# Kernel tuning notes

Measured on AMD Instinct MI355X. Metric: run time of the kernel, lower is better.

Reference implementation:

```python
import jax, jax.numpy as jnp
import numpy as np

V, D, M, H, C = 100000, 300, 300, 200, 5
L = 512


def setup_inputs() -> dict:
    key = jax.random.key(0)
    ks = jax.random.split(key, 20)
    def rn(k, shape, s=0.05):
        return jax.random.normal(k, shape, dtype=jnp.float32) * s
    return {
        "linputs": jax.random.randint(ks[0], (L,), 0, V),
        "rinputs": jax.random.randint(ks[1], (L,), 0, V),
        "emb": rn(ks[2], (V, D), 0.1),
        "ioux_w": rn(ks[3], (3 * M, D)), "ioux_b": jnp.zeros((3 * M,), jnp.float32),
        "iouh_w": rn(ks[4], (3 * M, M)), "iouh_b": jnp.zeros((3 * M,), jnp.float32),
        "fx_w": rn(ks[5], (M, D)), "fx_b": jnp.zeros((M,), jnp.float32),
        "fh_w": rn(ks[6], (M, M)), "fh_b": jnp.zeros((M,), jnp.float32),
        "Wa": rn(ks[7], (1, M)),
        "attnh_w": rn(ks[8], (M, 2 * M)), "attnh_b": jnp.zeros((M,), jnp.float32),
        "wh_w": rn(ks[9], (H, 4 * M)), "wh_b": jnp.zeros((H,), jnp.float32),
        "wp_w": rn(ks[10], (C, H)), "wp_b": jnp.zeros((C,), jnp.float32),
    }


def _run_chain(inputs, hmat, ioux_w, ioux_b, iouh_w, iouh_b, fx_w, fx_b, fh_w, fh_b,
               Wa, attnh_w, attnh_b):
    """Sequential ChildSum tree-LSTM chain (each node's sole child is the previous node).
    inputs: [L, D]; hmat: None or [N, M] attention memory. Returns (c, h, hs[L,M])."""
    m = iouh_w.shape[1]

    def step(carry, x):
        c, h = carry  # each [1, M]
        iou = (x @ ioux_w.T + ioux_b) + (h @ iouh_w.T + iouh_b)  # [1, 3M]
        i_, o_, u_ = jnp.split(iou, 3, axis=1)
        i_, o_, u_ = jax.nn.sigmoid(i_), jax.nn.sigmoid(o_), jnp.tanh(u_)
        f = jax.nn.sigmoid((h @ fh_w.T + fh_b) + (x @ fx_w.T + fx_b))  # [1, M]
        c_new = i_ * u_ + f * c  # sum over single child == identity
        h_new = o_ * jnp.tanh(c_new)
        if hmat is not None:
            n = hmat.shape[0]
            cat = jnp.concatenate([jnp.broadcast_to(h_new, (n, m)), hmat], axis=1)  # [N, 2M]
            scores = Wa @ jnp.tanh(cat @ attnh_w.T + attnh_b).T  # [1, N]
            s = jax.nn.softmax(scores, axis=1)  # [1, N]
            h_new = (jnp.sum((1.0 - s).T * hmat, axis=0, keepdims=True)
                     + jnp.sum(s.T * jnp.broadcast_to(h_new, (n, m)), axis=0, keepdims=True))
        return (c_new, h_new), h_new[0]

    init = (jnp.zeros((1, m), inputs.dtype), jnp.zeros((1, m), inputs.dtype))
    (c, h), hs = jax.lax.scan(step, init, inputs)
    return c, h, hs  # hs: [L, M]


def _forward(linputs, rinputs, emb, ioux_w, ioux_b, iouh_w, iouh_b, fx_w, fx_b,
             fh_w, fh_b, Wa, attnh_w, attnh_b, wh_w, wh_b, wp_w, wp_b):
    cell = (ioux_w, ioux_b, iouh_w, iouh_b, fx_w, fx_b, fh_w, fh_b, Wa, attnh_w, attnh_b)
    lemb = emb[linputs]          # [L, D]
    remb = emb[rinputs]          # [R, D]
    lflip = lemb[::-1]
    rflip = remb[::-1]

    # left, no attention (runs 1)
    _, lh_f1, hs_l_f = _run_chain(lemb, None, *cell)
    _, _, hs_l_b = _run_chain(lflip, None, *cell)
    lh_b1 = hs_l_b[0:1]
    lhidden_1 = jnp.concatenate([lh_f1, lh_b1], axis=1)  # [1, 2M]
    hs_l = jnp.tanh(hs_l_f + hs_l_b[::-1])               # [L, M]

    # right, attention over left hidden states
    _, rh_f1, _ = _run_chain(remb, hs_l, *cell)
    _, _, hs_tmp = _run_chain(rflip, hs_l, *cell)
    rh_b1 = hs_tmp[0:1]
    rhidden_1 = jnp.concatenate([rh_f1, rh_b1], axis=1)

    # right, no attention (runs 2)
    _, rh_f2, hs_r_f = _run_chain(remb, None, *cell)
    _, _, hs_r_b = _run_chain(rflip, None, *cell)
    rh_b2 = hs_r_b[0:1]
    rhidden_2 = jnp.concatenate([rh_f2, rh_b2], axis=1)
    hs_r = jnp.tanh(hs_r_f + hs_r_b[::-1])

    # left, attention over right hidden states
    _, lh_f2, _ = _run_chain(lemb, hs_r, *cell)
    _, _, hs_tmp2 = _run_chain(lflip, hs_r, *cell)
    lh_b2 = hs_tmp2[0:1]
    lhidden_2 = jnp.concatenate([lh_f2, lh_b2], axis=1)

    lhidden = jnp.tanh(lhidden_1 + lhidden_2)  # [1, 2M]
    rhidden = jnp.tanh(rhidden_1 + rhidden_2)

    mult_dist = lhidden * rhidden
    abs_dist = jnp.abs(lhidden - rhidden)
    vec_dist = jnp.concatenate([mult_dist, abs_dist], axis=1)  # [1, 4M]
    hid = jax.nn.sigmoid(vec_dist @ wh_w.T + wh_b)             # [1, H]
    return jax.nn.log_softmax(hid @ wp_w.T + wp_b, axis=1)     # [1, C]


def reference(linputs, rinputs, emb, ioux_w, ioux_b, iouh_w, iouh_b, fx_w, fx_b,
              fh_w, fh_b, Wa, attnh_w, attnh_b, wh_w, wh_b, wp_w, wp_b):
    return _forward(linputs, rinputs, emb, ioux_w, ioux_b, iouh_w, iouh_b,
                    fx_w, fx_b, fh_w, fh_b, Wa, attnh_w, attnh_b,
                    wh_w, wh_b, wp_w, wp_b)
```

## Files before the change

kernel.cpp:

```cpp
#include <hip/hip_runtime.h>
#include <hip/hip_bf16.h>

constexpr int kL = 512;
constexpr int kD = 300;
constexpr int kM = 300;
constexpr int NWG = 32;
constexpr int BLK = 256;
constexpr int JP = 10;
constexpr int NJW = 30;
constexpr int NSPLIT = 6;
constexpr int KLEN = 50;
constexpr int NSL = 16;
constexpr int SEG = 4;

constexpr int A_LEMB   = 1024;
constexpr int A_REMB   = A_LEMB   + kL*kD;
constexpr int A_XIOU_L = A_REMB   + kL*kD;
constexpr int A_XF_L   = A_XIOU_L + kL*900;
constexpr int A_XIOU_R = A_XF_L   + kL*300;
constexpr int A_XF_R   = A_XIOU_R + kL*900;
constexpr int A_HS_LF  = A_XF_R   + kL*300;
constexpr int A_HS_LB  = A_HS_LF  + kL*300;
constexpr int A_HS_RF  = A_HS_LB  + kL*300;
constexpr int A_HS_RB  = A_HS_RF  + kL*300;
constexpr int A_HS_L   = A_HS_RB  + kL*300;
constexpr int A_HS_R   = A_HS_L   + kL*300;
constexpr int A_HABUF  = A_HS_R   + kL*300;
constexpr int A_HBBUF  = A_HABUF  + 2400;
constexpr int A_HPACC  = A_HBBUF  + 2400;
constexpr int A_HACC   = A_HPACC  + 9600;
constexpr int A_DACC   = A_HACC   + 9600;
constexpr int A_BFIN   = A_DACC   + 256;
constexpr int A_END    = A_BFIN   + 1200;

__device__ __forceinline__ float fsig(float x) { return 1.0f / (1.0f + __expf(-x)); }
__device__ __forceinline__ float ftanh(float x) {
  x = fminf(fmaxf(x, -15.f), 15.f);
  float e = __expf(2.f * x);
  return (e - 1.f) / (e + 1.f);
}

__device__ __forceinline__ float aload(const float* p) {
  return __hip_atomic_load(p, __ATOMIC_RELAXED, __HIP_MEMORY_SCOPE_AGENT);
}
__device__ __forceinline__ void astore(float* p, float v) {
  __hip_atomic_store(p, v, __ATOMIC_RELAXED, __HIP_MEMORY_SCOPE_AGENT);
}

__device__ __forceinline__ void gbar(unsigned* ctr, int& epoch) {
  __syncthreads();
  if (threadIdx.x == 0) {
    ++epoch;
    __threadfence();
    atomicAdd(ctr, 1u);
    const unsigned tgt = (unsigned)(NWG * epoch);
    while (__hip_atomic_load(ctr, __ATOMIC_RELAXED, __HIP_MEMORY_SCOPE_AGENT) < tgt)
      __builtin_amdgcn_s_sleep(1);
    __threadfence();
  }
  __syncthreads();
}

__device__ __forceinline__ void gbar_fast(unsigned* ctr, int& epoch) {
  __syncthreads();
  if (threadIdx.x == 0) {
    ++epoch;
    atomicAdd(ctr, 1u);
    const unsigned tgt = (unsigned)(NWG * epoch);
    while (__hip_atomic_load(ctr, __ATOMIC_RELAXED, __HIP_MEMORY_SCOPE_AGENT) < tgt)
      __builtin_amdgcn_s_sleep(1);
  }
  __syncthreads();
}

__global__ __launch_bounds__(BLK) void treelstm_kernel(
    const int* __restrict__ linputs, const int* __restrict__ rinputs,
    const float* __restrict__ emb,
    const float* __restrict__ ioux_w, const float* __restrict__ ioux_b,
    const float* __restrict__ iouh_w, const float* __restrict__ iouh_b,
    const float* __restrict__ fx_w,  const float* __restrict__ fx_b,
    const float* __restrict__ fh_w,  const float* __restrict__ fh_b,
    const float* __restrict__ Wa,    const float* __restrict__ attnh_w,
    const float* __restrict__ attnh_b,
    const float* __restrict__ wh_w,  const float* __restrict__ wh_b,
    const float* __restrict__ wp_w,  const float* __restrict__ wp_b,
    float* __restrict__ ws, float* __restrict__ out) {

  __shared__ __align__(16) float h_lds[4][304];
  __shared__ __align__(16) float hpj_lds[4][304];
  __shared__ __align__(16) float part[4][40][6];
  __shared__ float gv[4][4][10];
  __shared__ float c_lds[4][10];
  __shared__ float hnew_lds[4][10];
  __shared__ float dred[4][32];
  __shared__ __align__(16) float colsum_lds[2][300];
  __shared__ float wa_lds[300];
  __shared__ float sc_lds[4][16];
  __shared__ float red_lds[32];
  __shared__ __align__(16) __hip_bfloat16 hmp_lds[2][NSL][300];
  __shared__ __align__(16) __hip_bfloat16 hmat_lds[2][NSL][300];
  __shared__ __hip_bfloat16 a1c_lds[JP][300];

  const int wg = blockIdx.x;
  const int tid = threadIdx.x;
  const int gthread = wg * BLK + tid;
  unsigned* ctr = (unsigned*)ws;
  float* W = ws;
  int epoch = 0;

  for (int i = gthread; i < 2 * kL * kD; i += NWG * BLK) {
    int side = i / (kL * kD); int r = i % (kL * kD); int t = r / kD; int d = r % kD;
    const int* idx = side ? rinputs : linputs;
    W[(side ? A_REMB : A_LEMB) + r] = emb[(long)idx[t] * kD + d];
  }
  for (int i = gthread; i < 4800; i += NWG * BLK) astore(&W[A_HABUF + i], 0.f);
  for (int i = gthread; i < 19200; i += NWG * BLK) astore(&W[A_HPACC + i], 0.f);
  gbar(ctr, epoch);

  for (int task = wg; task < 64; task += NWG) {
    int side = task & 1; int tb = task >> 1;
    float* xt = (float*)hmp_lds;
    const float* xbase = W + (side ? A_REMB : A_LEMB) + tb * 16 * kD;
    for (int i = tid; i < 16 * kD; i += BLK) xt[i] = xbase[i];
    __syncthreads();
    float* xiou = W + (side ? A_XIOU_R : A_XIOU_L) + tb * 16 * 900;
    float* xf   = W + (side ? A_XF_R   : A_XF_L)   + tb * 16 * 300;
    const float4* xt4 = (const float4*)xt;
    for (int id = tid; id < 1200; id += BLK) {
      int o4 = id >> 2, q = id & 3;
      int o0 = o4 * 4;
      float acc[4][4];
      const float* wrow[4]; float bias[4];
      #pragma unroll
      for (int m = 0; m < 4; ++m) {
        int o = o0 + m;
        if (o < 900) { wrow[m] = ioux_w + o * kD; bias[m] = ioux_b[o]; }
        else         { wrow[m] = fx_w + (o - 900) * kD; bias[m] = fx_b[o - 900]; }
        #pragma unroll
        for (int n = 0; n < 4; ++n) acc[m][n] = bias[m];
      }
      for (int k4 = 0; k4 < 75; ++k4) {
        float4 x4[4];
        #pragma unroll
        for (int n = 0; n < 4; ++n) x4[n] = xt4[(q * 4 + n) * 75 + k4];
        #pragma unroll
        for (int m = 0; m < 4; ++m) {
          float4 w4 = *(const float4*)(wrow[m] + k4 * 4);
          #pragma unroll
          for (int n = 0; n < 4; ++n)
            acc[m][n] += w4.x * x4[n].x + w4.y * x4[n].y + w4.z * x4[n].z + w4.w * x4[n].w;
        }
      }
      #pragma unroll
      for (int m = 0; m < 4; ++m) {
        int o = o0 + m;
        #pragma unroll
        for (int n = 0; n < 4; ++n) {
          int tt = q * 4 + n;
          if (o < 900) xiou[tt * 900 + o] = acc[m][n];
          else         xf[tt * 300 + (o - 900)] = acc[m][n];
        }
      }
    }
    __syncthreads();
  }
  gbar(ctr, epoch);

  float wreg[KLEN];
  int r6 = 0, s6 = 0, k0 = 0;
  if (wg < NJW && tid < 240) {
    r6 = tid / NSPLIT; s6 = tid % NSPLIT;
    int gate = r6 / JP, jl = r6 % JP, jg = wg * JP + jl;
    k0 = s6 * KLEN;
    const float* wrow = (gate < 3) ? (iouh_w + (gate * kM + jg) * kM) : (fh_w + jg * kM);
    #pragma unroll
    for (int k = 0; k < KLEN; ++k) wreg[k] = wrow[k0 + k];
  }
  float biasr = 0.f; int ach = 0, ag = 0, ajl = 0, ajg = 0;
  if (wg < NJW && tid < 160) {
    ach = tid / 40; ag = (tid / 10) % 4; ajl = tid % 10; ajg = wg * JP + ajl;
    biasr = (ag < 3) ? iouh_b[ag * kM + ajg] : fh_b[ajg];
  }
  int gch = 0, gjl = 0, gjg = 0;
  if (wg < NJW && tid < 40) { gch = tid / 10; gjl = tid % 10; gjg = wg * JP + gjl; }

  if (tid < 40) c_lds[tid / 10][tid % 10] = 0.f;
  __syncthreads();

  int p = 0;
  for (int t = 0; t < kL; ++t) {
    for (int i = tid; i < 1200; i += BLK)
      h_lds[i / 300][i % 300] = aload(&W[A_HABUF + p * 1200 + i]);
    float xv = 0.f;
    if (wg < NJW && tid < 160) {
      int trow = (ach & 1) ? (511 - t) : t;
      if (ag < 3) xv = W[(ach < 2 ? A_XIOU_L : A_XIOU_R) + trow * 900 + ag * 300 + ajg];
      else        xv = W[(ach < 2 ? A_XF_L   : A_XF_R)   + trow * 300 + ajg];
    }
    __syncthreads();
    if (wg < NJW && tid < 240) {
      #pragma unroll
      for (int ch = 0; ch < 4; ++ch) {
        float acc = 0.f;
        #pragma unroll
        for (int k = 0; k < KLEN; ++k) acc += wreg[k] * h_lds[ch][k0 + k];
        part[ch][r6][s6] = acc;
      }
    }
    __syncthreads();
    if (wg < NJW && tid < 160) {
      float pre = xv + biasr;
      #pragma unroll
      for (int s = 0; s < NSPLIT; ++s) pre += part[ach][ag * 10 + ajl][s];
      gv[ach][ag][ajl] = pre;
    }
    __syncthreads();
    if (wg < NJW && tid < 40) {
      float iv = fsig(gv[gch][0][gjl]);
      float ov = fsig(gv[gch][1][gjl]);
      float uv = ftanh(gv[gch][2][gjl]);
      float fv = fsig(gv[gch][3][gjl]);
      float c = iv * uv + fv * c_lds[gch][gjl];
      c_lds[gch][gjl] = c;
      float h = ov * ftanh(c);
      astore(&W[A_HABUF + (p ^ 1) * 1200 + gch * 300 + gjg], h);
      int hsoff = (gch == 0) ? A_HS_LF : (gch == 1) ? A_HS_LB : (gch == 2) ? A_HS_RF : A_HS_RB;
      astore(&W[hsoff + t * 300 + gjg], h);
    }
    gbar_fast(ctr, epoch);
    p ^= 1;
  }

  for (int i = gthread; i < 2 * kL * kM; i += NWG * BLK) {
    int side = i / (kL * kM); int r = i % (kL * kM); int n = r / kM; int j = r % kM;
    float v = ftanh(W[(side ? A_HS_RF : A_HS_LF) + n * kM + j] +
                    W[(side ? A_HS_RB : A_HS_LB) + (511 - n) * kM + j]);
    astore(&W[(side ? A_HS_R : A_HS_L) + n * kM + j], v);
  }
  gbar_fast(ctr, epoch);

  for (int j = tid; j < 300; j += BLK) wa_lds[j] = Wa[j];
  if (wg < NJW)
    for (int i = tid; i < JP * 300; i += BLK) {
      int kl = i / 300, j = i % 300;
      a1c_lds[kl][j] = __float2bfloat16(attnh_w[j * 600 + wg * JP + kl]);
    }
  for (int j = tid; j < 300; j += BLK) {
    float s0 = 0.f, s1 = 0.f;
    for (int n = 0; n < kL; ++n) { s0 += W[A_HS_L + n * 300 + j]; s1 += W[A_HS_R + n * 300 + j]; }
    colsum_lds[0][j] = s0; colsum_lds[1][j] = s1;
  }
  for (int side = 0; side < 2; ++side) {
    __syncthreads();
    float* stage = (float*)hmat_lds;
    for (int i = tid; i < NSL * 300; i += BLK)
      stage[i] = W[(side ? A_HS_R : A_HS_L) + (wg * NSL) * 300 + i];
    __syncthreads();
    const float4* st4 = (const float4*)stage;
    for (int id = tid; id < 1200; id += BLK) {
      int j = id >> 2, q = id & 3;
      float b = attnh_b[j];
      float acc[4] = {b, b, b, b};
      const float* wrow = attnh_w + j * 600 + 300;
      for (int k4 = 0; k4 < 75; ++k4) {
        float4 w4 = *(const float4*)(wrow + k4 * 4);
        #pragma unroll
        for (int m = 0; m < 4; ++m) {
          float4 x4 = st4[(q * 4 + m) * 75 + k4];
          acc[m] += w4.x * x4.x + w4.y * x4.y + w4.z * x4.z + w4.w * x4.w;
        }
      }
      #pragma unroll
      for (int m = 0; m < 4; ++m) hmp_lds[side][q * 4 + m][j] = __float2bfloat16(acc[m]);
    }
  }
  __syncthreads();
  for (int i = tid; i < 2 * NSL * 300; i += BLK) {
    int side = i / (NSL * 300); int r = i % (NSL * 300);
    hmat_lds[side][r / 300][r % 300] =
        __float2bfloat16(W[(side ? A_HS_R : A_HS_L) + (wg * NSL) * 300 + r]);
  }
  for (int i = tid; i < 1216; i += BLK) ((float*)h_lds)[i] = 0.f;
  if (tid < 40) c_lds[tid / 10][tid % 10] = 0.f;
  gbar_fast(ctr, epoch);

  int pb = 0;
  for (int t = 0; t < kL; ++t) {
    const int nact = (t == 0) ? 4 : 2;
    float xvb = 0.f;
    if (wg < NJW && tid < 160 && ach < nact) {
      int trow = (ach < 2) ? t : 511;
      int useL = ach & 1;
      if (ag < 3) xvb = W[(useL ? A_XIOU_L : A_XIOU_R) + trow * 900 + ag * 300 + ajg];
      else        xvb = W[(useL ? A_XF_L   : A_XF_R)   + trow * 300 + ajg];
    }
    __syncthreads();
    if (wg < NJW && tid < 240) {
      for (int ch = 0; ch < nact; ++ch) {
        float acc = 0.f;
        #pragma unroll
        for (int k = 0; k < KLEN; ++k) acc += wreg[k] * h_lds[ch][k0 + k];
        part[ch][r6][s6] = acc;
      }
    }
    __syncthreads();
    if (wg < NJW && tid < 160 && ach < nact) {
      float pre = xvb + biasr;
      #pragma unroll
      for (int s = 0; s < NSPLIT; ++s) pre += part[ach][ag * 10 + ajl][s];
      gv[ach][ag][ajl] = pre;
    }
    __syncthreads();
    if (wg < NJW && tid < 40 && gch < nact) {
      float iv = fsig(gv[gch][0][gjl]);
      float ov = fsig(gv[gch][1][gjl]);
      float uv = ftanh(gv[gch][2][gjl]);
      float fv = fsig(gv[gch][3][gjl]);
      float c = iv * uv + fv * c_lds[gch][gjl];
      c_lds[gch][gjl] = c;
      float h = ov * ftanh(c);
      astore(&W[A_HBBUF + pb * 1200 + gch * 300 + gjg], h);
      hnew_lds[gch][gjl] = h;
    }
    __syncthreads();
    if (wg < NJW) {
      for (int ch = 0; ch < nact; ++ch)
        for (int j = tid; j < 300; j += BLK) {
          float acc = 0.f;
          #pragma unroll
          for (int kl = 0; kl < JP; ++kl)
            acc += hnew_lds[ch][kl] * __bfloat162float(a1c_lds[kl][j]);
          atomicAdd(&W[A_HPACC + ((pb * SEG + (wg & 3)) * 4 + ch) * 300 + j], acc);
        }
    }
    gbar_fast(ctr, epoch);

    for (int i = tid; i < SEG * 4 * 300; i += BLK) astore(&W[A_HACC + (pb ^ 1) * 4800 + i], 0.f);
    for (int i = tid; i < nact * 300; i += BLK) {
      int ch = i / 300, j = i % 300;
      float s_ = 0.f;
      #pragma unroll
      for (int sg = 0; sg < SEG; ++sg) s_ += aload(&W[A_HPACC + ((pb * SEG + sg) * 4 + ch) * 300 + j]);
      hpj_lds[ch][j] = s_;
    }
    __syncthreads();
    float* pf = &part[0][0][0];
    for (int id = tid; id < nact * NSL * 8; id += BLK) {
      int ch = id / 128; int rem = id % 128; int nl = rem / 8; int js = rem % 8;
      int side = ch & 1;
      int j0 = js * 38; int j1 = j0 + 38; if (j1 > 300) j1 = 300;
      float acc = 0.f;
      for (int j = j0; j < j1; ++j)
        acc += wa_lds[j] * ftanh(hpj_lds[ch][j] + __bfloat162float(hmp_lds[side][nl][j]));
      pf[id] = acc;
    }
    __syncthreads();
    if (tid < nact * NSL) {
      int ch = tid / NSL, nl = tid % NSL;
      float sc = 0.f;
      #pragma unroll
      for (int js = 0; js < 8; ++js) sc += pf[(ch * NSL + nl) * 8 + js];
      sc = fminf(fmaxf(sc, -60.f), 60.f);
      sc_lds[ch][nl] = __expf(sc);
    }
    __syncthreads();
    if (tid < nact) {
      float dsum = 0.f;
      #pragma unroll
      for (int nl = 0; nl < NSL; ++nl) dsum += sc_lds[tid][nl];
      astore(&W[A_DACC + (pb * 32 + wg) * 4 + tid], dsum);
    }
    for (int ch = 0; ch < nact; ++ch) {
      int side = ch & 1;
      for (int j = tid; j < 300; j += BLK) {
        float acc = 0.f;
        #pragma unroll
        for (int nl = 0; nl < NSL; ++nl)
          acc += sc_lds[ch][nl] * __bfloat162float(hmat_lds[side][nl][j]);
        atomicAdd(&W[A_HACC + ((pb * SEG + (wg & 3)) * 4 + ch) * 300 + j], acc);
      }
    }
    gbar_fast(ctr, epoch);

    for (int i = tid; i < SEG * 4 * 300; i += BLK) astore(&W[A_HPACC + pb * 4800 + i], 0.f);
    if (tid < 32 * nact) {
      int ch = tid >> 5, w2 = tid & 31;
      dred[ch][w2] = aload(&W[A_DACC + (pb * 32 + w2) * 4 + ch]);
    }
    __syncthreads();
    if (tid < nact) {
      float den = 0.f;
      #pragma unroll
      for (int w2 = 0; w2 < NWG; ++w2) den += dred[tid][w2];
      gv[0][0][tid] = den;
    }
    __syncthreads();
    for (int ch = 0; ch < nact; ++ch) {
      float inv = 1.f / gv[0][0][ch];
      int side = ch & 1;
      for (int j = tid; j < 300; j += BLK) {
        float s_ = 0.f;
        #pragma unroll
        for (int sg = 0; sg < SEG; ++sg) s_ += aload(&W[A_HACC + ((pb * SEG + sg) * 4 + ch) * 300 + j]);
        float val = aload(&W[A_HBBUF + pb * 1200 + ch * 300 + j]) + colsum_lds[side][j] - s_ * inv;
        h_lds[ch][j] = val;
        if (t == 511 && ch == 0) astore(&W[A_BFIN + 0   + j], val);
        if (t == 511 && ch == 1) astore(&W[A_BFIN + 600 + j], val);
        if (t == 0   && ch == 2) astore(&W[A_BFIN + 300 + j], val);
        if (t == 0   && ch == 3) astore(&W[A_BFIN + 900 + j], val);
      }
    }
    __syncthreads();
    pb ^= 1;
  }
  gbar_fast(ctr, epoch);

  if (wg == 0) {
    float* hl = (float*)h_lds;
    float* vec = (float*)hpj_lds;
    float* hid = &part[0][0][0];
    for (int j = tid; j < 300; j += BLK) {
      float lf = W[A_HS_LF + 511 * 300 + j] + aload(&W[A_BFIN + 600 + j]);
      float lb = W[A_HS_LB + j]             + aload(&W[A_BFIN + 900 + j]);
      float rf = aload(&W[A_BFIN + j])      + W[A_HS_RF + 511 * 300 + j];
      float rb = aload(&W[A_BFIN + 300 + j]) + W[A_HS_RB + j];
      hl[j]        = ftanh(lf);
      hl[300 + j]  = ftanh(lb);
      hl[608 + j]  = ftanh(rf);
      hl[908 + j]  = ftanh(rb);
    }
    __syncthreads();
    for (int i = tid; i < 600; i += BLK) {
      float a = hl[i], b = hl[608 + i];
      vec[i] = a * b; vec[600 + i] = fabsf(a - b);
    }
    __syncthreads();
    for (int hh = tid; hh < 200; hh += BLK) {
      float acc = wh_b[hh];
      const float* wr = wh_w + hh * 1200;
      for (int i2 = 0; i2 < 1200; ++i2) acc += wr[i2] * vec[i2];
      hid[hh] = fsig(acc);
    }
    __syncthreads();
    if (tid < 5) {
      float acc = wp_b[tid];
      const float* wr = wp_w + tid * 200;
      for (int h2 = 0; h2 < 200; ++h2) acc += wr[h2] * hid[h2];
      red_lds[tid] = acc;
    }
    __syncthreads();
    if (tid == 0) {
      float mx = red_lds[0];
      for (int c2 = 1; c2 < 5; ++c2) mx = fmaxf(mx, red_lds[c2]);
      float se = 0.f;
      for (int c2 = 0; c2 < 5; ++c2) se += __expf(red_lds[c2] - mx);
      float lse = logf(se) + mx;
      for (int c2 = 0; c2 < 5; ++c2) out[c2] = red_lds[c2] - lse;
    }
  }
}

extern "C" void kernel_launch(void* const* d_in, const int* in_sizes, int n_in,
                              void* d_out, int out_size, void* d_ws, size_t ws_size,
                              hipStream_t stream) {
  (void)in_sizes; (void)n_in; (void)out_size; (void)ws_size;
  hipMemsetAsync(d_ws, 0, 256, stream);
  treelstm_kernel<<<NWG, BLK, 0, stream>>>(
      (const int*)d_in[0], (const int*)d_in[1], (const float*)d_in[2],
      (const float*)d_in[3], (const float*)d_in[4], (const float*)d_in[5],
      (const float*)d_in[6], (const float*)d_in[7], (const float*)d_in[8],
      (const float*)d_in[9], (const float*)d_in[10], (const float*)d_in[11],
      (const float*)d_in[12], (const float*)d_in[13], (const float*)d_in[14],
      (const float*)d_in[15], (const float*)d_in[16], (const float*)d_in[17],
      (float*)d_ws, (float*)d_out);
}
```

Before: 10.10 ms.

## Replace grid barriers with tagged-value dataflow polling in recurrent loops

```diff
diff --git a/kernel.cpp b/kernel.cpp
--- a/kernel.cpp
+++ b/kernel.cpp
@@ -11,7 +11,6 @@
 constexpr int NSPLIT = 6;
 constexpr int KLEN = 50;
 constexpr int NSL = 16;
-constexpr int SEG = 4;
 
 constexpr int A_LEMB   = 1024;
 constexpr int A_REMB   = A_LEMB   + kL*kD;
@@ -25,13 +24,15 @@
 constexpr int A_HS_RB  = A_HS_RF  + kL*300;
 constexpr int A_HS_L   = A_HS_RB  + kL*300;
 constexpr int A_HS_R   = A_HS_L   + kL*300;
-constexpr int A_HABUF  = A_HS_R   + kL*300;
-constexpr int A_HBBUF  = A_HABUF  + 2400;
-constexpr int A_HPACC  = A_HBBUF  + 2400;
-constexpr int A_HACC   = A_HPACC  + 9600;
-constexpr int A_DACC   = A_HACC   + 9600;
-constexpr int A_BFIN   = A_DACC   + 256;
-constexpr int A_END    = A_BFIN   + 1200;
+constexpr int A_TAIL   = A_HS_R   + kL*300;
+
+constexpr int U_PJ  = A_LEMB / 2;
+constexpr int U_PV  = U_PJ + 2*30*4*300;
+constexpr int U_HXA = A_TAIL / 2;
+constexpr int U_HXB = U_HXA + 2*4*300;
+constexpr int U_HP  = U_HXB + 2*2*300;
+constexpr int U_DEN = U_HP  + 2*4*300;
+constexpr int A_BFIN = (U_DEN + 2*32*4) * 2;
 
 __device__ __forceinline__ float fsig(float x) { return 1.0f / (1.0f + __expf(-x)); }
 __device__ __forceinline__ float ftanh(float x) {
@@ -45,6 +46,15 @@
 }
 __device__ __forceinline__ void astore(float* p, float v) {
   __hip_atomic_store(p, v, __ATOMIC_RELAXED, __HIP_MEMORY_SCOPE_AGENT);
+}
+__device__ __forceinline__ unsigned long long uload(const unsigned long long* p) {
+  return __hip_atomic_load(p, __ATOMIC_RELAXED, __HIP_MEMORY_SCOPE_AGENT);
+}
+__device__ __forceinline__ void ustore(unsigned long long* p, unsigned long long v) {
+  __hip_atomic_store(p, v, __ATOMIC_RELAXED, __HIP_MEMORY_SCOPE_AGENT);
+}
+__device__ __forceinline__ unsigned long long pack(unsigned tag, float v) {
+  return ((unsigned long long)tag << 32) | (unsigned long long)__float_as_uint(v);
 }
 
 __device__ __forceinline__ void gbar(unsigned* ctr, int& epoch) {
@@ -60,7 +70,6 @@
   }
   __syncthreads();
 }
-
 __device__ __forceinline__ void gbar_fast(unsigned* ctr, int& epoch) {
   __syncthreads();
   if (threadIdx.x == 0) {
@@ -71,6 +80,26 @@
       __builtin_amdgcn_s_sleep(1);
   }
   __syncthreads();
+}
+
+__device__ __forceinline__ void poll_lds(const unsigned long long* src, float* lds,
+                                         int n, unsigned tag) {
+  int idx[5]; int cnt = 0;
+  for (int i = threadIdx.x; i < n; i += BLK) idx[cnt++] = i;
+  int rem = cnt;
+  while (rem > 0) {
+    #pragma unroll
+    for (int q = 0; q < 5; ++q) {
+      if (q < cnt && idx[q] >= 0) {
+        unsigned long long v = uload(&src[idx[q]]);
+        if ((unsigned)(v >> 32) == tag) {
+          int i = idx[q];
+          lds[(i / 300) * 304 + (i % 300)] = __uint_as_float((unsigned)v);
+          idx[q] = -1; --rem;
+        }
+      }
+    }
+  }
 }
 
 __global__ __launch_bounds__(BLK) void treelstm_kernel(
@@ -106,6 +135,8 @@
   const int gthread = wg * BLK + tid;
   unsigned* ctr = (unsigned*)ws;
   float* W = ws;
+  unsigned long long* Ux = (unsigned long long*)ws;
+  float (*part2)[6] = (float(*)[6])&part[0][0][0];
   int epoch = 0;
 
   for (int i = gthread; i < 2 * kL * kD; i += NWG * BLK) {
@@ -113,8 +144,8 @@
     const int* idx = side ? rinputs : linputs;
     W[(side ? A_REMB : A_LEMB) + r] = emb[(long)idx[t] * kD + d];
   }
-  for (int i = gthread; i < 4800; i += NWG * BLK) astore(&W[A_HABUF + i], 0.f);
-  for (int i = gthread; i < 19200; i += NWG * BLK) astore(&W[A_HPACC + i], 0.f);
+  for (int i = gthread; i < 1200; i += NWG * BLK)
+    ustore(&Ux[U_HXA + i], pack(0u, 0.f));
   gbar(ctr, epoch);
 
   for (int task = wg; task < 64; task += NWG) {
@@ -187,49 +218,49 @@
   if (tid < 40) c_lds[tid / 10][tid % 10] = 0.f;
   __syncthreads();
 
-  int p = 0;
-  for (int t = 0; t < kL; ++t) {
-    for (int i = tid; i < 1200; i += BLK)
-      h_lds[i / 300][i % 300] = aload(&W[A_HABUF + p * 1200 + i]);
-    float xv = 0.f;
-    if (wg < NJW && tid < 160) {
-      int trow = (ach & 1) ? (511 - t) : t;
-      if (ag < 3) xv = W[(ach < 2 ? A_XIOU_L : A_XIOU_R) + trow * 900 + ag * 300 + ajg];
-      else        xv = W[(ach < 2 ? A_XF_L   : A_XF_R)   + trow * 300 + ajg];
-    }
-    __syncthreads();
-    if (wg < NJW && tid < 240) {
-      #pragma unroll
-      for (int ch = 0; ch < 4; ++ch) {
-        float acc = 0.f;
-        #pragma unroll
-        for (int k = 0; k < KLEN; ++k) acc += wreg[k] * h_lds[ch][k0 + k];
-        part[ch][r6][s6] = acc;
-      }
-    }
-    __syncthreads();
-    if (wg < NJW && tid < 160) {
-      float pre = xv + biasr;
-      #pragma unroll
-      for (int s = 0; s < NSPLIT; ++s) pre += part[ach][ag * 10 + ajl][s];
-      gv[ach][ag][ajl] = pre;
-    }
-    __syncthreads();
-    if (wg < NJW && tid < 40) {
-      float iv = fsig(gv[gch][0][gjl]);
-      float ov = fsig(gv[gch][1][gjl]);
-      float uv = ftanh(gv[gch][2][gjl]);
-      float fv = fsig(gv[gch][3][gjl]);
-      float c = iv * uv + fv * c_lds[gch][gjl];
-      c_lds[gch][gjl] = c;
-      float h = ov * ftanh(c);
-      astore(&W[A_HABUF + (p ^ 1) * 1200 + gch * 300 + gjg], h);
-      int hsoff = (gch == 0) ? A_HS_LF : (gch == 1) ? A_HS_LB : (gch == 2) ? A_HS_RF : A_HS_RB;
-      astore(&W[hsoff + t * 300 + gjg], h);
-    }
-    gbar_fast(ctr, epoch);
-    p ^= 1;
-  }
+  if (wg < NJW) {
+    for (int t = 0; t < kL; ++t) {
+      float xv = 0.f;
+      if (tid < 160) {
+        int trow = (ach & 1) ? (511 - t) : t;
+        if (ag < 3) xv = W[(ach < 2 ? A_XIOU_L : A_XIOU_R) + trow * 900 + ag * 300 + ajg];
+        else        xv = W[(ach < 2 ? A_XF_L   : A_XF_R)   + trow * 300 + ajg];
+      }
+      poll_lds(&Ux[U_HXA + (t & 1) * 1200], &h_lds[0][0], 1200, (unsigned)t);
+      __syncthreads();
+      if (tid < 240) {
+        #pragma unroll
+        for (int ch = 0; ch < 4; ++ch) {
+          float acc = 0.f;
+          #pragma unroll
+          for (int k = 0; k < KLEN; ++k) acc += wreg[k] * h_lds[ch][k0 + k];
+          part[ch][r6][s6] = acc;
+        }
+      }
+      __syncthreads();
+      if (tid < 160) {
+        float pre = xv + biasr;
+        #pragma unroll
+        for (int s = 0; s < NSPLIT; ++s) pre += part[ach][ag * 10 + ajl][s];
+        gv[ach][ag][ajl] = pre;
+      }
+      __syncthreads();
+      if (tid < 40) {
+        float iv = fsig(gv[gch][0][gjl]);
+        float ov = fsig(gv[gch][1][gjl]);
+        float uv = ftanh(gv[gch][2][gjl]);
+        float fv = fsig(gv[gch][3][gjl]);
+        float c = iv * uv + fv * c_lds[gch][gjl];
+        c_lds[gch][gjl] = c;
+        float h = ov * ftanh(c);
+        ustore(&Ux[U_HXA + ((t + 1) & 1) * 1200 + gch * 300 + gjg],
+               pack((unsigned)(t + 1), h));
+        int hsoff = (gch == 0) ? A_HS_LF : (gch == 1) ? A_HS_LB : (gch == 2) ? A_HS_RF : A_HS_RB;
+        astore(&W[hsoff + t * 300 + gjg], h);
+      }
+    }
+  }
+  gbar_fast(ctr, epoch);
 
   for (int i = gthread; i < 2 * kL * kM; i += NWG * BLK) {
     int side = i / (kL * kM); int r = i % (kL * kM); int n = r / kM; int j = r % kM;
@@ -280,69 +311,93 @@
     hmat_lds[side][r / 300][r % 300] =
         __float2bfloat16(W[(side ? A_HS_R : A_HS_L) + (wg * NSL) * 300 + r]);
   }
-  for (int i = tid; i < 1216; i += BLK) ((float*)h_lds)[i] = 0.f;
   if (tid < 40) c_lds[tid / 10][tid % 10] = 0.f;
   gbar_fast(ctr, epoch);
 
-  int pb = 0;
   for (int t = 0; t < kL; ++t) {
     const int nact = (t == 0) ? 4 : 2;
-    float xvb = 0.f;
-    if (wg < NJW && tid < 160 && ach < nact) {
-      int trow = (ach < 2) ? t : 511;
-      int useL = ach & 1;
-      if (ag < 3) xvb = W[(useL ? A_XIOU_L : A_XIOU_R) + trow * 900 + ag * 300 + ajg];
-      else        xvb = W[(useL ? A_XF_L   : A_XF_R)   + trow * 300 + ajg];
-    }
-    __syncthreads();
-    if (wg < NJW && tid < 240) {
-      for (int ch = 0; ch < nact; ++ch) {
-        float acc = 0.f;
-        #pragma unroll
-        for (int k = 0; k < KLEN; ++k) acc += wreg[k] * h_lds[ch][k0 + k];
-        part[ch][r6][s6] = acc;
-      }
-    }
-    __syncthreads();
-    if (wg < NJW && tid < 160 && ach < nact) {
-      float pre = xvb + biasr;
-      #pragma unroll
-      for (int s = 0; s < NSPLIT; ++s) pre += part[ach][ag * 10 + ajl][s];
-      gv[ach][ag][ajl] = pre;
-    }
-    __syncthreads();
-    if (wg < NJW && tid < 40 && gch < nact) {
-      float iv = fsig(gv[gch][0][gjl]);
-      float ov = fsig(gv[gch][1][gjl]);
-      float uv = ftanh(gv[gch][2][gjl]);
-      float fv = fsig(gv[gch][3][gjl]);
-      float c = iv * uv + fv * c_lds[gch][gjl];
-      c_lds[gch][gjl] = c;
-      float h = ov * ftanh(c);
-      astore(&W[A_HBBUF + pb * 1200 + gch * 300 + gjg], h);
-      hnew_lds[gch][gjl] = h;
-    }
-    __syncthreads();
+    const unsigned tagS = (unsigned)(t + 1);
+    const int rows = nact * JP;
+    const int sl = t & 1;
+
     if (wg < NJW) {
-      for (int ch = 0; ch < nact; ++ch)
-        for (int j = tid; j < 300; j += BLK) {
+      float xvb = 0.f;
+      if (tid < 160 && ach < nact) {
+        int trow = (ach < 2) ? t : 511;
+        int useL = ach & 1;
+        if (ag < 3) xvb = W[(useL ? A_XIOU_L : A_XIOU_R) + trow * 900 + ag * 300 + ajg];
+        else        xvb = W[(useL ? A_XF_L   : A_XF_R)   + trow * 300 + ajg];
+      }
+      if (t == 0) {
+        for (int i = tid; i < 1216; i += BLK) ((float*)h_lds)[i] = 0.f;
+      } else {
+        poll_lds(&Ux[U_HXB + sl * 600], &h_lds[0][0], 600, (unsigned)t);
+      }
+      __syncthreads();
+      if (tid < 240) {
+        for (int ch = 0; ch < nact; ++ch) {
           float acc = 0.f;
           #pragma unroll
-          for (int kl = 0; kl < JP; ++kl)
-            acc += hnew_lds[ch][kl] * __bfloat162float(a1c_lds[kl][j]);
-          atomicAdd(&W[A_HPACC + ((pb * SEG + (wg & 3)) * 4 + ch) * 300 + j], acc);
-        }
-    }
-    gbar_fast(ctr, epoch);
-
-    for (int i = tid; i < SEG * 4 * 300; i += BLK) astore(&W[A_HACC + (pb ^ 1) * 4800 + i], 0.f);
-    for (int i = tid; i < nact * 300; i += BLK) {
-      int ch = i / 300, j = i % 300;
-      float s_ = 0.f;
-      #pragma unroll
-      for (int sg = 0; sg < SEG; ++sg) s_ += aload(&W[A_HPACC + ((pb * SEG + sg) * 4 + ch) * 300 + j]);
-      hpj_lds[ch][j] = s_;
-    }
+          for (int k = 0; k < KLEN; ++k) acc += wreg[k] * h_lds[ch][k0 + k];
+          part[ch][r6][s6] = acc;
+        }
+      }
+      __syncthreads();
+      if (tid < 160 && ach < nact) {
+        float pre = xvb + biasr;
+        #pragma unroll
+        for (int s = 0; s < NSPLIT; ++s) pre += part[ach][ag * 10 + ajl][s];
+        gv[ach][ag][ajl] = pre;
+      }
+      __syncthreads();
+      if (tid < 40 && gch < nact) {
+        float iv = fsig(gv[gch][0][gjl]);
+        float ov = fsig(gv[gch][1][gjl]);
+        float uv = ftanh(gv[gch][2][gjl]);
+        float fv = fsig(gv[gch][3][gjl]);
+        float c = iv * uv + fv * c_lds[gch][gjl];
+        c_lds[gch][gjl] = c;
+        hnew_lds[gch][gjl] = ov * ftanh(c);
+      }
+      __syncthreads();
+      for (int i = tid; i < nact * 300; i += BLK) {
+        int ch = i / 300, j = i % 300;
+        float acc = 0.f;
+        #pragma unroll
+        for (int kl = 0; kl < JP; ++kl)
+          acc += hnew_lds[ch][kl] * __bfloat162float(a1c_lds[kl][j]);
+        ustore(&Ux[U_PJ + sl * 36000 + wg * 1200 + ch * 300 + j], pack(tagS, acc));
+      }
+      if (tid < rows * 6) {
+        int r = tid / 6, l = tid % 6;
+        int ch = r / JP, jl = r % JP, jg = wg * JP + jl;
+        float acc = 0.f; unsigned pend = 0x1fu;
+        while (pend) {
+          #pragma unroll
+          for (int k = 0; k < 5; ++k) {
+            if (pend & (1u << k)) {
+              unsigned long long v =
+                  uload(&Ux[U_PJ + sl * 36000 + (l * 5 + k) * 1200 + ch * 300 + jg]);
+              if ((unsigned)(v >> 32) == tagS) {
+                acc += __uint_as_float((unsigned)v);
+                pend &= ~(1u << k);
+              }
+            }
+          }
+        }
+        part2[r][l] = acc;
+      }
+      __syncthreads();
+      if (tid < rows) {
+        float hp = 0.f;
+        #pragma unroll
+        for (int l = 0; l < 6; ++l) hp += part2[tid][l];
+        int ch = tid / JP, jl = tid % JP;
+        ustore(&Ux[U_HP + sl * 1200 + ch * 300 + wg * JP + jl], pack(tagS, hp));
+      }
+    }
+
+    poll_lds(&Ux[U_HP + sl * 1200], &hpj_lds[0][0], nact * 300, tagS);
     __syncthreads();
     float* pf = &part[0][0][0];
     for (int id = tid; id < nact * NSL * 8; id += BLK) {
@@ -368,50 +423,77 @@
       float dsum = 0.f;
       #pragma unroll
       for (int nl = 0; nl < NSL; ++nl) dsum += sc_lds[tid][nl];
-      astore(&W[A_DACC + (pb * 32 + wg) * 4 + tid], dsum);
-    }
-    for (int ch = 0; ch < nact; ++ch) {
+      ustore(&Ux[U_DEN + sl * 128 + wg * 4 + tid], pack(tagS, dsum));
+    }
+    for (int i = tid; i < nact * 300; i += BLK) {
+      int ch = i / 300, j = i % 300;
       int side = ch & 1;
-      for (int j = tid; j < 300; j += BLK) {
-        float acc = 0.f;
-        #pragma unroll
-        for (int nl = 0; nl < NSL; ++nl)
-          acc += sc_lds[ch][nl] * __bfloat162float(hmat_lds[side][nl][j]);
-        atomicAdd(&W[A_HACC + ((pb * SEG + (wg & 3)) * 4 + ch) * 300 + j], acc);
-      }
-    }
-    gbar_fast(ctr, epoch);
-
-    for (int i = tid; i < SEG * 4 * 300; i += BLK) astore(&W[A_HPACC + pb * 4800 + i], 0.f);
-    if (tid < 32 * nact) {
-      int ch = tid >> 5, w2 = tid & 31;
-      dred[ch][w2] = aload(&W[A_DACC + (pb * 32 + w2) * 4 + ch]);
-    }
-    __syncthreads();
-    if (tid < nact) {
-      float den = 0.f;
+      float acc = 0.f;
       #pragma unroll
-      for (int w2 = 0; w2 < NWG; ++w2) den += dred[tid][w2];
-      gv[0][0][tid] = den;
-    }
-    __syncthreads();
-    for (int ch = 0; ch < nact; ++ch) {
-      float inv = 1.f / gv[0][0][ch];
-      int side = ch & 1;
-      for (int j = tid; j < 300; j += BLK) {
+      for (int nl = 0; nl < NSL; ++nl)
+        acc += sc_lds[ch][nl] * __bfloat162float(hmat_lds[side][nl][j]);
+      ustore(&Ux[U_PV + sl * 38400 + wg * 1200 + ch * 300 + j], pack(tagS, acc));
+    }
+
+    if (wg < NJW) {
+      if (tid < rows * 6) {
+        int r = tid / 6, l = tid % 6;
+        int ch = r / JP, jl = r % JP, jg = wg * JP + jl;
+        float acc = 0.f; unsigned pend = 0u;
+        #pragma unroll
+        for (int k = 0; k < 6; ++k) if (l * 6 + k < 32) pend |= (1u << k);
+        while (pend) {
+          #pragma unroll
+          for (int k = 0; k < 6; ++k) {
+            if (pend & (1u << k)) {
+              unsigned long long v =
+                  uload(&Ux[U_PV + sl * 38400 + (l * 6 + k) * 1200 + ch * 300 + jg]);
+              if ((unsigned)(v >> 32) == tagS) {
+                acc += __uint_as_float((unsigned)v);
+                pend &= ~(1u << k);
+              }
+            }
+          }
+        }
+        part2[r][l] = acc;
+      } else if (tid >= 240) {
+        int q = tid - 240;
+        unsigned pend = 0u;
+        #pragma unroll
+        for (int k = 0; k < 8; ++k) if (((q * 8 + k) & 3) < nact) pend |= (1u << k);
+        while (pend) {
+          #pragma unroll
+          for (int k = 0; k < 8; ++k) {
+            if (pend & (1u << k)) {
+              int idx = q * 8 + k;
+              unsigned long long v = uload(&Ux[U_DEN + sl * 128 + idx]);
+              if ((unsigned)(v >> 32) == tagS) {
+                dred[idx & 3][idx >> 2] = __uint_as_float((unsigned)v);
+                pend &= ~(1u << k);
+              }
+            }
+          }
+        }
+      }
+      __syncthreads();
+      if (tid < rows) {
+        int ch = tid / JP, jl = tid % JP, jg = wg * JP + jl;
         float s_ = 0.f;
         #pragma unroll
-        for (int sg = 0; sg < SEG; ++sg) s_ += aload(&W[A_HACC + ((pb * SEG + sg) * 4 + ch) * 300 + j]);
-        float val = aload(&W[A_HBBUF + pb * 1200 + ch * 300 + j]) + colsum_lds[side][j] - s_ * inv;
-        h_lds[ch][j] = val;
-        if (t == 511 && ch == 0) astore(&W[A_BFIN + 0   + j], val);
-        if (t == 511 && ch == 1) astore(&W[A_BFIN + 600 + j], val);
-        if (t == 0   && ch == 2) astore(&W[A_BFIN + 300 + j], val);
-        if (t == 0   && ch == 3) astore(&W[A_BFIN + 900 + j], val);
-      }
-    }
-    __syncthreads();
-    pb ^= 1;
+        for (int l = 0; l < 6; ++l) s_ += part2[tid][l];
+        float den = 0.f;
+        #pragma unroll
+        for (int w2 = 0; w2 < 32; ++w2) den += dred[ch][w2];
+        float val = hnew_lds[ch][jl] + colsum_lds[ch & 1][jg] - s_ / den;
+        if (ch < 2) {
+          if (t < 511) ustore(&Ux[U_HXB + ((t + 1) & 1) * 600 + ch * 300 + jg],
+                              pack((unsigned)(t + 1), val));
+          else astore(&W[A_BFIN + (ch ? 600 : 0) + jg], val);
+        } else {
+          astore(&W[A_BFIN + (ch == 2 ? 300 : 900) + jg], val);
+        }
+      }
+    }
   }
   gbar_fast(ctr, epoch);
 
```

Result: faster. 9.695 ms (-4.0%).
